# Performance work log

Measured on AMD Instinct MI355X. Metric: run time of the kernel, lower is better.

Reference implementation:

```python
import jax, jax.numpy as jnp
import numpy as np

B, H, W, C = 4, 64, 64, 512
DQK = C // 8


def setup_inputs() -> dict:
    key = jax.random.key(0)
    k1, k2, k3, k4 = jax.random.split(key, 4)
    x = jax.random.normal(k1, (B, H, W, C), dtype=jnp.float32)
    kernel_f = jax.random.normal(k2, (1, 1, C, DQK), dtype=jnp.float32) * 0.02
    kernel_g = jax.random.normal(k3, (1, 1, C, DQK), dtype=jnp.float32) * 0.02
    kernel_h = jax.random.normal(k4, (1, 1, C, C), dtype=jnp.float32) * 0.02
    gamma = jnp.ones((1,), dtype=jnp.float32)  # nonzero so attention branch contributes
    return {"x": x, "kernel_f": kernel_f, "kernel_g": kernel_g,
            "kernel_h": kernel_h, "gamma": gamma}


def reference(x, kernel_f, kernel_g, kernel_h, gamma):
    b, h, w, c = x.shape
    n = h * w
    xt = x.reshape(b, n, c)  # 1x1 conv == per-pixel matmul
    f = jnp.einsum('bnc,cd->bnd', xt, kernel_f[0, 0])       # [b,n,dqk]
    g = jnp.einsum('bnc,cd->bnd', xt, kernel_g[0, 0])       # [b,n,dqk]
    v = jnp.einsum('bnc,cd->bnd', xt, kernel_h[0, 0])       # [b,n,c]
    s = jnp.einsum('bid,bjd->bij', f, g)                    # [b,n,n] = f @ g^T
    beta = jax.nn.softmax(s, axis=-1)
    out = jnp.einsum('bij,bjc->bic', beta, v)               # [b,n,c]
    out = out.reshape(b, h, w, c)
    return gamma * out + x
```

## Files before the change

kernel.cpp:

```cpp
#include <hip/hip_runtime.h>


typedef __bf16 bf16x8 __attribute__((ext_vector_type(8)));
typedef __bf16 bf16x2 __attribute__((ext_vector_type(2)));
typedef float f32x4 __attribute__((ext_vector_type(4)));
typedef unsigned int u32x4 __attribute__((ext_vector_type(4)));
typedef unsigned int u32;

#define L2E 1.4426950408889634f

__device__ __forceinline__ unsigned short f2bf(float f) {
    unsigned int u = __builtin_bit_cast(unsigned int, f);
    u += 0x7fffu + ((u >> 16) & 1u);
    return (unsigned short)(u >> 16);
}
__device__ __forceinline__ u32 cvtpk(float a, float b) {
    bf16x2 t; t[0] = (__bf16)a; t[1] = (__bf16)b;
    return __builtin_bit_cast(u32, t);
}
__device__ __forceinline__ bf16x8 ld8(const void* p) {
    u32x4 u = *reinterpret_cast<const u32x4*>(p);
    return __builtin_bit_cast(bf16x8, u);
}
__device__ __forceinline__ bf16x8 ldx(const float* p) {
    float4 a = *reinterpret_cast<const float4*>(p);
    float4 b = *reinterpret_cast<const float4*>(p + 4);
    u32x4 r;
    r.x = cvtpk(a.x, a.y); r.y = cvtpk(a.z, a.w);
    r.z = cvtpk(b.x, b.y); r.w = cvtpk(b.z, b.w);
    return __builtin_bit_cast(bf16x8, r);
}
__device__ __forceinline__ f32x4 mfma16(bf16x8 a, bf16x8 b, f32x4 c) {
    return __builtin_amdgcn_mfma_f32_16x16x32_bf16(a, b, c, 0, 0, 0);
}
__device__ __forceinline__ void gl2lds16(const void* g, void* l) {
    __builtin_amdgcn_global_load_lds(
        (const __attribute__((address_space(1))) u32*)g,
        (__attribute__((address_space(3))) u32*)l, 16, 0, 0);
}

__global__ __launch_bounds__(256) void cvt_w_all(const float* __restrict__ kf,
                                                 const float* __restrict__ kg,
                                                 const float* __restrict__ kh,
                                                 unsigned short* __restrict__ wst) {
    int idx = blockIdx.x * 256 + threadIdx.x;
    int j = idx & 7;
    int gi = idx >> 3;
    int c = gi % 640;
    int sq = gi / 640;
    int k = (sq >> 2) * 32 + (sq & 3) * 8 + j;
    float v;
    if (c < 64)       v = kf[k * 64 + c] * L2E;
    else if (c < 128) v = kg[k * 64 + (c - 64)];
    else              v = kh[k * 512 + (c - 128)];
    wst[idx] = f2bf(v);
}

__global__ __launch_bounds__(256, 2) void proj_k(const float* __restrict__ x,
                                                 const unsigned short* __restrict__ wst,
                                                 unsigned short* __restrict__ fq,
                                                 unsigned short* __restrict__ kst,
                                                 unsigned short* __restrict__ vst) {
    __shared__ __align__(16) unsigned char Wl[2][20480];
    __shared__ unsigned short Tl[64][72];

    int m0 = blockIdx.x * 64;
    int grp = blockIdx.y;
    int tid = threadIdx.x;
    int w = tid >> 6, l = tid & 63, g = l >> 4, i = l & 15;

    const char* wsrc = (const char*)wst + (size_t)w * 10240 + (size_t)grp * 5120 + l * 16;

#pragma unroll
    for (int s5 = 0; s5 < 5; s5++)
        gl2lds16(wsrc + s5 * 1024, &Wl[0][w * 5120 + s5 * 1024]);

    const float* xrow = x + (size_t)(m0 + 16 * w + i) * 512 + g * 8;
    bf16x8 af[16];
#pragma unroll
    for (int k = 0; k < 16; k++) af[k] = ldx(xrow + 32 * k);

    f32x4 acc[5][4];
#pragma unroll
    for (int t = 0; t < 5; t++)
#pragma unroll
        for (int cf = 0; cf < 4; cf++) acc[t][cf] = f32x4{0, 0, 0, 0};

    int rdoff = g * 5120 + i * 16;

#pragma unroll
    for (int q = 0; q < 16; q++) {
        __syncthreads();
        if (q < 15) {
            const char* src = wsrc + (size_t)(q + 1) * 40960;
#pragma unroll
            for (int s5 = 0; s5 < 5; s5++)
                gl2lds16(src + s5 * 1024, &Wl[(q + 1) & 1][w * 5120 + s5 * 1024]);
        }
        const unsigned char* Wb = &Wl[q & 1][0];
        __builtin_amdgcn_s_setprio(1);
#pragma unroll
        for (int t = 0; t < 5; t++)
#pragma unroll
            for (int cf = 0; cf < 4; cf++) {
                bf16x8 bb = ld8(Wb + rdoff + (t * 64 + 16 * cf) * 16);
                acc[t][cf] = mfma16(af[q], bb, acc[t][cf]);
            }
        __builtin_amdgcn_s_setprio(0);
    }

    int batch = m0 >> 12;
    int kt = (m0 & 4095) >> 6;
    unsigned short* kbase = kst + (size_t)batch * 262144 + (size_t)kt * 4096;
    unsigned short* vbase = vst + (size_t)batch * 2097152 + (size_t)kt * 32768;

#pragma unroll
    for (int t = 0; t < 5; t++) {
        if (grp == 0 && t == 0) {
#pragma unroll
            for (int cf = 0; cf < 4; cf++)
#pragma unroll
                for (int r = 0; r < 4; r++)
                    fq[(size_t)(m0 + 16 * w + 4 * g + r) * 64 + 16 * cf + i] =
                        f2bf(acc[t][cf][r]);
        } else {
            __syncthreads();
#pragma unroll
            for (int cf = 0; cf < 4; cf++) {
                ushort4 v4;
                v4.x = f2bf(acc[t][cf][0]); v4.y = f2bf(acc[t][cf][1]);
                v4.z = f2bf(acc[t][cf][2]); v4.w = f2bf(acc[t][cf][3]);
                *reinterpret_cast<ushort4*>(&Tl[16 * cf + i][16 * w + 4 * g]) = v4;
            }
            __syncthreads();
            if (grp == 0 && t == 1) {
#pragma unroll
                for (int ch = tid; ch < 512; ch += 256) {
                    int jf2 = ch >> 7, ks = (ch >> 6) & 1, l2 = ch & 63;
                    int g2 = l2 >> 4, i2 = l2 & 15;
                    ushort4 o0, o1;
                    o0.x = Tl[ks * 32 + 8 * g2 + 0][16 * jf2 + i2];
                    o0.y = Tl[ks * 32 + 8 * g2 + 1][16 * jf2 + i2];
                    o0.z = Tl[ks * 32 + 8 * g2 + 2][16 * jf2 + i2];
                    o0.w = Tl[ks * 32 + 8 * g2 + 3][16 * jf2 + i2];
                    o1.x = Tl[ks * 32 + 8 * g2 + 4][16 * jf2 + i2];
                    o1.y = Tl[ks * 32 + 8 * g2 + 5][16 * jf2 + i2];
                    o1.z = Tl[ks * 32 + 8 * g2 + 6][16 * jf2 + i2];
                    o1.w = Tl[ks * 32 + 8 * g2 + 7][16 * jf2 + i2];
                    unsigned short* dst = kbase + (size_t)(jf2 * 1024 + ks * 512 + l2 * 8);
                    *reinterpret_cast<ushort4*>(dst)     = o0;
                    *reinterpret_cast<ushort4*>(dst + 4) = o1;
                }
            } else {
                int n0 = (grp == 0) ? (t - 2) * 64 : 192 + t * 64;
#pragma unroll
                for (int ch = tid; ch < 512; ch += 256) {
                    int cc = ch >> 7, ks = (ch >> 6) & 1, l2 = ch & 63;
                    int g2 = l2 >> 4, i2 = l2 & 15;
                    int row = cc * 16 + i2;
                    int jb = 32 * ks + 4 * g2;
                    ushort4 o0, o1;
                    o0.x = Tl[row][jb + 0];  o0.y = Tl[row][jb + 1];
                    o0.z = Tl[row][jb + 2];  o0.w = Tl[row][jb + 3];
                    o1.x = Tl[row][jb + 16]; o1.y = Tl[row][jb + 17];
                    o1.z = Tl[row][jb + 18]; o1.w = Tl[row][jb + 19];
                    int c16 = (n0 >> 4) + cc;
                    unsigned short* dst = vbase + (size_t)(c16 * 1024 + ks * 512 + l2 * 8);
                    *reinterpret_cast<ushort4*>(dst)     = o0;
                    *reinterpret_cast<ushort4*>(dst + 4) = o1;
                }
            }
        }
    }
}

__global__ __launch_bounds__(512, 2) void attn_k(const unsigned short* __restrict__ fq,
                                                 const unsigned short* __restrict__ kst,
                                                 const unsigned short* __restrict__ vst,
                                                 const float* __restrict__ x,
                                                 const float* __restrict__ gamma,
                                                 float* __restrict__ out) {
    __shared__ __align__(16) unsigned char Pl[4][8192];
    __shared__ float l_lds[64];

    int bid = blockIdx.x;
    int xcd = bid & 7;
    int batch = xcd >> 1;
    int qidx = ((xcd & 1) << 5) | (bid >> 3);
    int q0 = qidx * 64;

    int tid = threadIdx.x;
    int w = tid >> 6, l = tid & 63, g = l >> 4, i = l & 15;
    int jf = w >> 1, qfh = w & 1;

    if (tid < 64) l_lds[tid] = 0.0f;

    const unsigned short* fqb = fq + (size_t)batch * 4096 * 64;
    const char* kb = (const char*)kst + (size_t)batch * 524288;
    const char* vb = (const char*)vst + (size_t)batch * 4194304;

    bf16x8 aQ[2][2];
#pragma unroll
    for (int qf_l = 0; qf_l < 2; qf_l++)
#pragma unroll
        for (int ks = 0; ks < 2; ks++)
            aQ[qf_l][ks] = ld8(fqb + (size_t)(q0 + 16 * (2 * qfh + qf_l) + i) * 64 +
                               ks * 32 + g * 8);

    f32x4 acc[4][4];
#pragma unroll
    for (int a = 0; a < 4; a++)
#pragma unroll
        for (int b = 0; b < 4; b++) acc[a][b] = f32x4{0, 0, 0, 0};
    float lp[2] = {0.0f, 0.0f};

    int pwoff = ((2 * qfh) * 2 + (jf >> 1)) * 1024 + l * 16 + (jf & 1) * 8;
    int c16w = w * 4;

    bf16x8 kAa[2], kAb[2];
    kAa[0] = ld8(kb + (size_t)jf * 2048 + l * 16);
    kAa[1] = ld8(kb + (size_t)jf * 2048 + 1024 + l * 16);
    kAb[0] = ld8(kb + (size_t)(4 + jf) * 2048 + l * 16);
    kAb[1] = ld8(kb + (size_t)(4 + jf) * 2048 + 1024 + l * 16);

    bf16x8 vbr_a[4][2], vbr_b[4][2];
#pragma unroll
    for (int cf = 0; cf < 4; cf++)
#pragma unroll
        for (int ks = 0; ks < 2; ks++) {
            vbr_a[cf][ks] = ld8(vb + (size_t)(c16w + cf) * 2048 + ks * 1024 + l * 16);
            vbr_b[cf][ks] = ld8(vb + (size_t)(32 + c16w + cf) * 2048 + ks * 1024 + l * 16);
        }

    {
        f32x4 s0[2] = {f32x4{0,0,0,0}, f32x4{0,0,0,0}};
        f32x4 s1[2] = {f32x4{0,0,0,0}, f32x4{0,0,0,0}};
#pragma unroll
        for (int qf_l = 0; qf_l < 2; qf_l++) {
            s0[qf_l] = mfma16(kAa[0], aQ[qf_l][0], s0[qf_l]);
            s0[qf_l] = mfma16(kAa[1], aQ[qf_l][1], s0[qf_l]);
            s1[qf_l] = mfma16(kAb[0], aQ[qf_l][0], s1[qf_l]);
            s1[qf_l] = mfma16(kAb[1], aQ[qf_l][1], s1[qf_l]);
        }
        kAa[0] = ld8(kb + (size_t)(8 + jf) * 2048 + l * 16);
        kAa[1] = ld8(kb + (size_t)(8 + jf) * 2048 + 1024 + l * 16);
        kAb[0] = ld8(kb + (size_t)(12 + jf) * 2048 + l * 16);
        kAb[1] = ld8(kb + (size_t)(12 + jf) * 2048 + 1024 + l * 16);
#pragma unroll
        for (int qf_l = 0; qf_l < 2; qf_l++) {
            float p0 = __builtin_amdgcn_exp2f(s0[qf_l][0]);
            float p1 = __builtin_amdgcn_exp2f(s0[qf_l][1]);
            float p2 = __builtin_amdgcn_exp2f(s0[qf_l][2]);
            float p3 = __builtin_amdgcn_exp2f(s0[qf_l][3]);
            lp[qf_l] += (p0 + p1) + (p2 + p3);
            uint2 pk2; pk2.x = cvtpk(p0, p1); pk2.y = cvtpk(p2, p3);
            *reinterpret_cast<uint2*>(&Pl[0][0] + pwoff + qf_l * 2048) = pk2;
            p0 = __builtin_amdgcn_exp2f(s1[qf_l][0]);
            p1 = __builtin_amdgcn_exp2f(s1[qf_l][1]);
            p2 = __builtin_amdgcn_exp2f(s1[qf_l][2]);
            p3 = __builtin_amdgcn_exp2f(s1[qf_l][3]);
            lp[qf_l] += (p0 + p1) + (p2 + p3);
            pk2.x = cvtpk(p0, p1); pk2.y = cvtpk(p2, p3);
            *reinterpret_cast<uint2*>(&Pl[1][0] + pwoff + qf_l * 2048) = pk2;
        }
    }

    for (int u = 0; u < 32; ++u) {
        asm volatile("s_waitcnt lgkmcnt(0)" ::: "memory");
        __builtin_amdgcn_s_barrier();

        const unsigned char* Pr0 = &Pl[(u & 1) * 2][0];
        const unsigned char* Pr1 = Pr0 + 8192;

        f32x4 s0[2] = {f32x4{0,0,0,0}, f32x4{0,0,0,0}};
        f32x4 s1[2] = {f32x4{0,0,0,0}, f32x4{0,0,0,0}};
#pragma unroll
        for (int qf_l = 0; qf_l < 2; qf_l++) {
            s0[qf_l] = mfma16(kAa[0], aQ[qf_l][0], s0[qf_l]);
            s0[qf_l] = mfma16(kAa[1], aQ[qf_l][1], s0[qf_l]);
            s1[qf_l] = mfma16(kAb[0], aQ[qf_l][0], s1[qf_l]);
            s1[qf_l] = mfma16(kAb[1], aQ[qf_l][1], s1[qf_l]);
        }

        {
            int ta = (2 * u + 4) & 63, tb = (2 * u + 5) & 63;
            const char* ka = kb + (size_t)(ta * 4 + jf) * 2048;
            const char* kp = kb + (size_t)(tb * 4 + jf) * 2048;
            kAa[0] = ld8(ka + l * 16);
            kAa[1] = ld8(ka + 1024 + l * 16);
            kAb[0] = ld8(kp + l * 16);
            kAb[1] = ld8(kp + 1024 + l * 16);
        }

        {
            bf16x8 aP[4][2];
#pragma unroll
            for (int qf = 0; qf < 4; qf++)
#pragma unroll
                for (int ks = 0; ks < 2; ks++)
                    aP[qf][ks] = ld8(Pr0 + (qf * 2 + ks) * 1024 + l * 16);
            __builtin_amdgcn_s_setprio(1);
#pragma unroll
            for (int cf = 0; cf < 4; cf++)
#pragma unroll
                for (int qf = 0; qf < 4; qf++) {
                    acc[qf][cf] = mfma16(aP[qf][0], vbr_a[cf][0], acc[qf][cf]);
                    acc[qf][cf] = mfma16(aP[qf][1], vbr_a[cf][1], acc[qf][cf]);
                }
            __builtin_amdgcn_s_setprio(0);
        }
        {
            int tv = (2 * u + 2) & 63;
#pragma unroll
            for (int cf = 0; cf < 4; cf++)
#pragma unroll
                for (int ks = 0; ks < 2; ks++)
                    vbr_a[cf][ks] = ld8(vb + (size_t)(tv * 32 + c16w + cf) * 2048 +
                                        ks * 1024 + l * 16);
        }

        {
            bf16x8 aP[4][2];
#pragma unroll
            for (int qf = 0; qf < 4; qf++)
#pragma unroll
                for (int ks = 0; ks < 2; ks++)
                    aP[qf][ks] = ld8(Pr1 + (qf * 2 + ks) * 1024 + l * 16);
            __builtin_amdgcn_s_setprio(1);
#pragma unroll
            for (int cf = 0; cf < 4; cf++)
#pragma unroll
                for (int qf = 0; qf < 4; qf++) {
                    acc[qf][cf] = mfma16(aP[qf][0], vbr_b[cf][0], acc[qf][cf]);
                    acc[qf][cf] = mfma16(aP[qf][1], vbr_b[cf][1], acc[qf][cf]);
                }
            __builtin_amdgcn_s_setprio(0);
        }
        {
            int tv = (2 * u + 3) & 63;
#pragma unroll
            for (int cf = 0; cf < 4; cf++)
#pragma unroll
                for (int ks = 0; ks < 2; ks++)
                    vbr_b[cf][ks] = ld8(vb + (size_t)(tv * 32 + c16w + cf) * 2048 +
                                        ks * 1024 + l * 16);
        }

        float msk = (u < 31) ? 1.0f : 0.0f;
        unsigned char* Pw0 = &Pl[((u + 1) & 1) * 2][0];
        unsigned char* Pw1 = Pw0 + 8192;
#pragma unroll
        for (int qf_l = 0; qf_l < 2; qf_l++) {
            float p0 = __builtin_amdgcn_exp2f(s0[qf_l][0]);
            float p1 = __builtin_amdgcn_exp2f(s0[qf_l][1]);
            float p2 = __builtin_amdgcn_exp2f(s0[qf_l][2]);
            float p3 = __builtin_amdgcn_exp2f(s0[qf_l][3]);
            lp[qf_l] += msk * ((p0 + p1) + (p2 + p3));
            uint2 pk2; pk2.x = cvtpk(p0, p1); pk2.y = cvtpk(p2, p3);
            *reinterpret_cast<uint2*>(Pw0 + pwoff + qf_l * 2048) = pk2;
            p0 = __builtin_amdgcn_exp2f(s1[qf_l][0]);
            p1 = __builtin_amdgcn_exp2f(s1[qf_l][1]);
            p2 = __builtin_amdgcn_exp2f(s1[qf_l][2]);
            p3 = __builtin_amdgcn_exp2f(s1[qf_l][3]);
            lp[qf_l] += msk * ((p0 + p1) + (p2 + p3));
            pk2.x = cvtpk(p0, p1); pk2.y = cvtpk(p2, p3);
            *reinterpret_cast<uint2*>(Pw1 + pwoff + qf_l * 2048) = pk2;
        }
    }

#pragma unroll
    for (int qf_l = 0; qf_l < 2; qf_l++) {
        lp[qf_l] += __shfl_xor(lp[qf_l], 16, 64);
        lp[qf_l] += __shfl_xor(lp[qf_l], 32, 64);
    }
    if (g == 0) {
        atomicAdd(&l_lds[16 * (2 * qfh + 0) + i], lp[0]);
        atomicAdd(&l_lds[16 * (2 * qfh + 1) + i], lp[1]);
    }
    __syncthreads();

    float gam = gamma[0];
#pragma unroll
    for (int qf = 0; qf < 4; qf++) {
#pragma unroll
        for (int r = 0; r < 4; r++) {
            float linv = gam / l_lds[16 * qf + 4 * g + r];
            int n = q0 + 16 * qf + 4 * g + r;
            size_t base = ((size_t)batch * 4096 + n) * 512 + 64 * w;
#pragma unroll
            for (int cf = 0; cf < 4; cf++)
                out[base + 16 * cf + i] = acc[qf][cf][r] * linv + x[base + 16 * cf + i];
        }
    }
}


extern "C" void kernel_launch(void* const* d_in, const int* in_sizes, int n_in,
                              void* d_out, int out_size, void* d_ws, size_t ws_size,
                              hipStream_t stream) {
    const float* x = (const float*)d_in[0];
    const float* kf = (const float*)d_in[1];
    const float* kg = (const float*)d_in[2];
    const float* kh = (const float*)d_in[3];
    const float* gamma = (const float*)d_in[4];
    float* out = (float*)d_out;

    char* ws = (char*)d_ws;
    unsigned short* Fq  = (unsigned short*)(ws);
    unsigned short* Kst = (unsigned short*)(ws + 2097152);
    unsigned short* Vst = (unsigned short*)(ws + 4194304);
    unsigned short* Wst = (unsigned short*)(ws + 20971520);

    cvt_w_all<<<1280, 256, 0, stream>>>(kf, kg, kh, Wst);
    proj_k<<<dim3(256, 2), 256, 0, stream>>>(x, Wst, Fq, Kst, Vst);
    attn_k<<<256, 512, 0, stream>>>(Fq, Kst, Vst, x, gamma, out);
}
```

Baseline: 109.8 us.

## Split attention waves into QK/softmax producers and PV consumers

The attention kernel now gives waves 0-3 the job of computing the QK^T scores, exp and row sums, writing P into double-buffered LDS. Waves 4-7 do only the P·V MFMAs over 128 channels each and write the epilogue. The aim is to let softmax and score work overlap with the PV matrix work on different waves, instead of interleaving them in every wave. In exchange, each consumer wave holds a 4x8 accumulator tile plus a single V register buffer that is reloaded right after use. Under the launch bounds this could cause register spills or expose V load latency, and producer and consumer workloads are unbalanced.

```diff
diff --git a/kernel.cpp b/kernel.cpp
--- a/kernel.cpp
+++ b/kernel.cpp
@@ -121,7 +121,7 @@
             for (int cf = 0; cf < 4; cf++)
 #pragma unroll
                 for (int r = 0; r < 4; r++)
-                    fq[(size_t)(m0 + 16 * w + 4 * g + r) * 64 + 16 * cf + i] =
+                    fq[(size_t)(m0 + 16 * w + 4 * g + r) * 64 + t * 64 + 16 * cf + i] =
                         f2bf(acc[t][cf][r]);
         } else {
             __syncthreads();
@@ -191,205 +191,209 @@
 
     int tid = threadIdx.x;
     int w = tid >> 6, l = tid & 63, g = l >> 4, i = l & 15;
-    int jf = w >> 1, qfh = w & 1;
-
-    if (tid < 64) l_lds[tid] = 0.0f;
 
     const unsigned short* fqb = fq + (size_t)batch * 4096 * 64;
     const char* kb = (const char*)kst + (size_t)batch * 524288;
     const char* vb = (const char*)vst + (size_t)batch * 4194304;
 
-    bf16x8 aQ[2][2];
-#pragma unroll
-    for (int qf_l = 0; qf_l < 2; qf_l++)
+    if (w < 4) {
+        int qf = w;
+        bf16x8 aQ[2];
 #pragma unroll
         for (int ks = 0; ks < 2; ks++)
-            aQ[qf_l][ks] = ld8(fqb + (size_t)(q0 + 16 * (2 * qfh + qf_l) + i) * 64 +
-                               ks * 32 + g * 8);
-
-    f32x4 acc[4][4];
-#pragma unroll
-    for (int a = 0; a < 4; a++)
-#pragma unroll
-        for (int b = 0; b < 4; b++) acc[a][b] = f32x4{0, 0, 0, 0};
-    float lp[2] = {0.0f, 0.0f};
-
-    int pwoff = ((2 * qfh) * 2 + (jf >> 1)) * 1024 + l * 16 + (jf & 1) * 8;
-    int c16w = w * 4;
-
-    bf16x8 kAa[2], kAb[2];
-    kAa[0] = ld8(kb + (size_t)jf * 2048 + l * 16);
-    kAa[1] = ld8(kb + (size_t)jf * 2048 + 1024 + l * 16);
-    kAb[0] = ld8(kb + (size_t)(4 + jf) * 2048 + l * 16);
-    kAb[1] = ld8(kb + (size_t)(4 + jf) * 2048 + 1024 + l * 16);
-
-    bf16x8 vbr_a[4][2], vbr_b[4][2];
-#pragma unroll
-    for (int cf = 0; cf < 4; cf++)
-#pragma unroll
-        for (int ks = 0; ks < 2; ks++) {
-            vbr_a[cf][ks] = ld8(vb + (size_t)(c16w + cf) * 2048 + ks * 1024 + l * 16);
-            vbr_b[cf][ks] = ld8(vb + (size_t)(32 + c16w + cf) * 2048 + ks * 1024 + l * 16);
-        }
-
-    {
-        f32x4 s0[2] = {f32x4{0,0,0,0}, f32x4{0,0,0,0}};
-        f32x4 s1[2] = {f32x4{0,0,0,0}, f32x4{0,0,0,0}};
-#pragma unroll
-        for (int qf_l = 0; qf_l < 2; qf_l++) {
-            s0[qf_l] = mfma16(kAa[0], aQ[qf_l][0], s0[qf_l]);
-            s0[qf_l] = mfma16(kAa[1], aQ[qf_l][1], s0[qf_l]);
-            s1[qf_l] = mfma16(kAb[0], aQ[qf_l][0], s1[qf_l]);
-            s1[qf_l] = mfma16(kAb[1], aQ[qf_l][1], s1[qf_l]);
-        }
-        kAa[0] = ld8(kb + (size_t)(8 + jf) * 2048 + l * 16);
-        kAa[1] = ld8(kb + (size_t)(8 + jf) * 2048 + 1024 + l * 16);
-        kAb[0] = ld8(kb + (size_t)(12 + jf) * 2048 + l * 16);
-        kAb[1] = ld8(kb + (size_t)(12 + jf) * 2048 + 1024 + l * 16);
-#pragma unroll
-        for (int qf_l = 0; qf_l < 2; qf_l++) {
-            float p0 = __builtin_amdgcn_exp2f(s0[qf_l][0]);
-            float p1 = __builtin_amdgcn_exp2f(s0[qf_l][1]);
-            float p2 = __builtin_amdgcn_exp2f(s0[qf_l][2]);
-            float p3 = __builtin_amdgcn_exp2f(s0[qf_l][3]);
-            lp[qf_l] += (p0 + p1) + (p2 + p3);
-            uint2 pk2; pk2.x = cvtpk(p0, p1); pk2.y = cvtpk(p2, p3);
-            *reinterpret_cast<uint2*>(&Pl[0][0] + pwoff + qf_l * 2048) = pk2;
-            p0 = __builtin_amdgcn_exp2f(s1[qf_l][0]);
-            p1 = __builtin_amdgcn_exp2f(s1[qf_l][1]);
-            p2 = __builtin_amdgcn_exp2f(s1[qf_l][2]);
-            p3 = __builtin_amdgcn_exp2f(s1[qf_l][3]);
-            lp[qf_l] += (p0 + p1) + (p2 + p3);
-            pk2.x = cvtpk(p0, p1); pk2.y = cvtpk(p2, p3);
-            *reinterpret_cast<uint2*>(&Pl[1][0] + pwoff + qf_l * 2048) = pk2;
-        }
-    }
-
-    for (int u = 0; u < 32; ++u) {
-        asm volatile("s_waitcnt lgkmcnt(0)" ::: "memory");
-        __builtin_amdgcn_s_barrier();
-
-        const unsigned char* Pr0 = &Pl[(u & 1) * 2][0];
-        const unsigned char* Pr1 = Pr0 + 8192;
-
-        f32x4 s0[2] = {f32x4{0,0,0,0}, f32x4{0,0,0,0}};
-        f32x4 s1[2] = {f32x4{0,0,0,0}, f32x4{0,0,0,0}};
-#pragma unroll
-        for (int qf_l = 0; qf_l < 2; qf_l++) {
-            s0[qf_l] = mfma16(kAa[0], aQ[qf_l][0], s0[qf_l]);
-            s0[qf_l] = mfma16(kAa[1], aQ[qf_l][1], s0[qf_l]);
-            s1[qf_l] = mfma16(kAb[0], aQ[qf_l][0], s1[qf_l]);
-            s1[qf_l] = mfma16(kAb[1], aQ[qf_l][1], s1[qf_l]);
-        }
+            aQ[ks] = ld8(fqb + (size_t)(q0 + 16 * qf + i) * 64 + ks * 32 + g * 8);
+
+        bf16x8 kAa[4][2], kAb[4][2];
+#pragma unroll
+        for (int jf = 0; jf < 4; jf++)
+#pragma unroll
+            for (int ks = 0; ks < 2; ks++) {
+                kAa[jf][ks] = ld8(kb + (size_t)(0 * 4 + jf) * 2048 + ks * 1024 + l * 16);
+                kAb[jf][ks] = ld8(kb + (size_t)(1 * 4 + jf) * 2048 + ks * 1024 + l * 16);
+            }
+
+        float lp = 0.0f;
+        int pw[4];
+#pragma unroll
+        for (int jf = 0; jf < 4; jf++)
+            pw[jf] = (qf * 2 + (jf >> 1)) * 1024 + l * 16 + (jf & 1) * 8;
 
         {
-            int ta = (2 * u + 4) & 63, tb = (2 * u + 5) & 63;
-            const char* ka = kb + (size_t)(ta * 4 + jf) * 2048;
-            const char* kp = kb + (size_t)(tb * 4 + jf) * 2048;
-            kAa[0] = ld8(ka + l * 16);
-            kAa[1] = ld8(ka + 1024 + l * 16);
-            kAb[0] = ld8(kp + l * 16);
-            kAb[1] = ld8(kp + 1024 + l * 16);
-        }
-
-        {
-            bf16x8 aP[4][2];
-#pragma unroll
-            for (int qf = 0; qf < 4; qf++)
-#pragma unroll
-                for (int ks = 0; ks < 2; ks++)
-                    aP[qf][ks] = ld8(Pr0 + (qf * 2 + ks) * 1024 + l * 16);
-            __builtin_amdgcn_s_setprio(1);
-#pragma unroll
-            for (int cf = 0; cf < 4; cf++)
-#pragma unroll
-                for (int qf = 0; qf < 4; qf++) {
-                    acc[qf][cf] = mfma16(aP[qf][0], vbr_a[cf][0], acc[qf][cf]);
-                    acc[qf][cf] = mfma16(aP[qf][1], vbr_a[cf][1], acc[qf][cf]);
+            f32x4 s0[4], s1[4];
+#pragma unroll
+            for (int jf = 0; jf < 4; jf++) { s0[jf] = f32x4{0,0,0,0}; s1[jf] = f32x4{0,0,0,0}; }
+#pragma unroll
+            for (int jf = 0; jf < 4; jf++) {
+                s0[jf] = mfma16(kAa[jf][0], aQ[0], s0[jf]);
+                s0[jf] = mfma16(kAa[jf][1], aQ[1], s0[jf]);
+                s1[jf] = mfma16(kAb[jf][0], aQ[0], s1[jf]);
+                s1[jf] = mfma16(kAb[jf][1], aQ[1], s1[jf]);
+            }
+#pragma unroll
+            for (int jf = 0; jf < 4; jf++)
+#pragma unroll
+                for (int ks = 0; ks < 2; ks++) {
+                    kAa[jf][ks] = ld8(kb + (size_t)(2 * 4 + jf) * 2048 + ks * 1024 + l * 16);
+                    kAb[jf][ks] = ld8(kb + (size_t)(3 * 4 + jf) * 2048 + ks * 1024 + l * 16);
                 }
-            __builtin_amdgcn_s_setprio(0);
-        }
-        {
-            int tv = (2 * u + 2) & 63;
-#pragma unroll
-            for (int cf = 0; cf < 4; cf++)
-#pragma unroll
-                for (int ks = 0; ks < 2; ks++)
-                    vbr_a[cf][ks] = ld8(vb + (size_t)(tv * 32 + c16w + cf) * 2048 +
-                                        ks * 1024 + l * 16);
-        }
-
-        {
-            bf16x8 aP[4][2];
-#pragma unroll
-            for (int qf = 0; qf < 4; qf++)
-#pragma unroll
-                for (int ks = 0; ks < 2; ks++)
-                    aP[qf][ks] = ld8(Pr1 + (qf * 2 + ks) * 1024 + l * 16);
-            __builtin_amdgcn_s_setprio(1);
-#pragma unroll
-            for (int cf = 0; cf < 4; cf++)
-#pragma unroll
-                for (int qf = 0; qf < 4; qf++) {
-                    acc[qf][cf] = mfma16(aP[qf][0], vbr_b[cf][0], acc[qf][cf]);
-                    acc[qf][cf] = mfma16(aP[qf][1], vbr_b[cf][1], acc[qf][cf]);
+#pragma unroll
+            for (int jf = 0; jf < 4; jf++) {
+                float p0 = __builtin_amdgcn_exp2f(s0[jf][0]);
+                float p1 = __builtin_amdgcn_exp2f(s0[jf][1]);
+                float p2 = __builtin_amdgcn_exp2f(s0[jf][2]);
+                float p3 = __builtin_amdgcn_exp2f(s0[jf][3]);
+                lp += (p0 + p1) + (p2 + p3);
+                uint2 pk2; pk2.x = cvtpk(p0, p1); pk2.y = cvtpk(p2, p3);
+                *reinterpret_cast<uint2*>(&Pl[0][0] + pw[jf]) = pk2;
+                p0 = __builtin_amdgcn_exp2f(s1[jf][0]);
+                p1 = __builtin_amdgcn_exp2f(s1[jf][1]);
+                p2 = __builtin_amdgcn_exp2f(s1[jf][2]);
+                p3 = __builtin_amdgcn_exp2f(s1[jf][3]);
+                lp += (p0 + p1) + (p2 + p3);
+                pk2.x = cvtpk(p0, p1); pk2.y = cvtpk(p2, p3);
+                *reinterpret_cast<uint2*>(&Pl[1][0] + pw[jf]) = pk2;
+            }
+        }
+
+        for (int u = 0; u < 32; ++u) {
+            asm volatile("s_waitcnt lgkmcnt(0)" ::: "memory");
+            __builtin_amdgcn_s_barrier();
+
+            f32x4 s0[4], s1[4];
+#pragma unroll
+            for (int jf = 0; jf < 4; jf++) { s0[jf] = f32x4{0,0,0,0}; s1[jf] = f32x4{0,0,0,0}; }
+#pragma unroll
+            for (int jf = 0; jf < 4; jf++) {
+                s0[jf] = mfma16(kAa[jf][0], aQ[0], s0[jf]);
+                s0[jf] = mfma16(kAa[jf][1], aQ[1], s0[jf]);
+                s1[jf] = mfma16(kAb[jf][0], aQ[0], s1[jf]);
+                s1[jf] = mfma16(kAb[jf][1], aQ[1], s1[jf]);
+            }
+
+            {
+                int ta = (2 * u + 4) & 63, tb = (2 * u + 5) & 63;
+#pragma unroll
+                for (int jf = 0; jf < 4; jf++)
+#pragma unroll
+                    for (int ks = 0; ks < 2; ks++) {
+                        kAa[jf][ks] = ld8(kb + (size_t)(ta * 4 + jf) * 2048 + ks * 1024 + l * 16);
+                        kAb[jf][ks] = ld8(kb + (size_t)(tb * 4 + jf) * 2048 + ks * 1024 + l * 16);
+                    }
+            }
+
+            float msk = (u < 31) ? 1.0f : 0.0f;
+            unsigned char* Pw0 = &Pl[((u + 1) & 1) * 2][0];
+            unsigned char* Pw1 = Pw0 + 8192;
+#pragma unroll
+            for (int jf = 0; jf < 4; jf++) {
+                float p0 = __builtin_amdgcn_exp2f(s0[jf][0]);
+                float p1 = __builtin_amdgcn_exp2f(s0[jf][1]);
+                float p2 = __builtin_amdgcn_exp2f(s0[jf][2]);
+                float p3 = __builtin_amdgcn_exp2f(s0[jf][3]);
+                lp += msk * ((p0 + p1) + (p2 + p3));
+                uint2 pk2; pk2.x = cvtpk(p0, p1); pk2.y = cvtpk(p2, p3);
+                *reinterpret_cast<uint2*>(Pw0 + pw[jf]) = pk2;
+                p0 = __builtin_amdgcn_exp2f(s1[jf][0]);
+                p1 = __builtin_amdgcn_exp2f(s1[jf][1]);
+                p2 = __builtin_amdgcn_exp2f(s1[jf][2]);
+                p3 = __builtin_amdgcn_exp2f(s1[jf][3]);
+                lp += msk * ((p0 + p1) + (p2 + p3));
+                pk2.x = cvtpk(p0, p1); pk2.y = cvtpk(p2, p3);
+                *reinterpret_cast<uint2*>(Pw1 + pw[jf]) = pk2;
+            }
+        }
+
+        lp += __shfl_xor(lp, 16, 64);
+        lp += __shfl_xor(lp, 32, 64);
+        if (g == 0) l_lds[16 * qf + i] = lp;
+        __syncthreads();
+    } else {
+        int p = w - 4;
+        int c16b = 8 * p;
+
+        bf16x8 vbr[8][2];
+#pragma unroll
+        for (int cf = 0; cf < 8; cf++)
+#pragma unroll
+            for (int ks = 0; ks < 2; ks++)
+                vbr[cf][ks] = ld8(vb + (size_t)(c16b + cf) * 2048 + ks * 1024 + l * 16);
+
+        f32x4 acc[4][8];
+#pragma unroll
+        for (int a = 0; a < 4; a++)
+#pragma unroll
+            for (int b = 0; b < 8; b++) acc[a][b] = f32x4{0, 0, 0, 0};
+
+        for (int u = 0; u < 32; ++u) {
+            asm volatile("s_waitcnt lgkmcnt(0)" ::: "memory");
+            __builtin_amdgcn_s_barrier();
+
+            const unsigned char* Pr0 = &Pl[(u & 1) * 2][0];
+            const unsigned char* Pr1 = Pr0 + 8192;
+
+            {
+                bf16x8 aP[4][2];
+#pragma unroll
+                for (int qf = 0; qf < 4; qf++)
+#pragma unroll
+                    for (int ks = 0; ks < 2; ks++)
+                        aP[qf][ks] = ld8(Pr0 + (qf * 2 + ks) * 1024 + l * 16);
+                int tv = (2 * u + 1) & 63;
+                __builtin_amdgcn_s_setprio(1);
+#pragma unroll
+                for (int cf = 0; cf < 8; cf++) {
+#pragma unroll
+                    for (int qf = 0; qf < 4; qf++) {
+                        acc[qf][cf] = mfma16(aP[qf][0], vbr[cf][0], acc[qf][cf]);
+                        acc[qf][cf] = mfma16(aP[qf][1], vbr[cf][1], acc[qf][cf]);
+                    }
+#pragma unroll
+                    for (int ks = 0; ks < 2; ks++)
+                        vbr[cf][ks] = ld8(vb + (size_t)(tv * 32 + c16b + cf) * 2048 +
+                                          ks * 1024 + l * 16);
                 }
-            __builtin_amdgcn_s_setprio(0);
-        }
-        {
-            int tv = (2 * u + 3) & 63;
-#pragma unroll
-            for (int cf = 0; cf < 4; cf++)
-#pragma unroll
-                for (int ks = 0; ks < 2; ks++)
-                    vbr_b[cf][ks] = ld8(vb + (size_t)(tv * 32 + c16w + cf) * 2048 +
-                                        ks * 1024 + l * 16);
-        }
-
-        float msk = (u < 31) ? 1.0f : 0.0f;
-        unsigned char* Pw0 = &Pl[((u + 1) & 1) * 2][0];
-        unsigned char* Pw1 = Pw0 + 8192;
-#pragma unroll
-        for (int qf_l = 0; qf_l < 2; qf_l++) {
-            float p0 = __builtin_amdgcn_exp2f(s0[qf_l][0]);
-            float p1 = __builtin_amdgcn_exp2f(s0[qf_l][1]);
-            float p2 = __builtin_amdgcn_exp2f(s0[qf_l][2]);
-            float p3 = __builtin_amdgcn_exp2f(s0[qf_l][3]);
-            lp[qf_l] += msk * ((p0 + p1) + (p2 + p3));
-            uint2 pk2; pk2.x = cvtpk(p0, p1); pk2.y = cvtpk(p2, p3);
-            *reinterpret_cast<uint2*>(Pw0 + pwoff + qf_l * 2048) = pk2;
-            p0 = __builtin_amdgcn_exp2f(s1[qf_l][0]);
-            p1 = __builtin_amdgcn_exp2f(s1[qf_l][1]);
-            p2 = __builtin_amdgcn_exp2f(s1[qf_l][2]);
-            p3 = __builtin_amdgcn_exp2f(s1[qf_l][3]);
-            lp[qf_l] += msk * ((p0 + p1) + (p2 + p3));
-            pk2.x = cvtpk(p0, p1); pk2.y = cvtpk(p2, p3);
-            *reinterpret_cast<uint2*>(Pw1 + pwoff + qf_l * 2048) = pk2;
-        }
-    }
-
-#pragma unroll
-    for (int qf_l = 0; qf_l < 2; qf_l++) {
-        lp[qf_l] += __shfl_xor(lp[qf_l], 16, 64);
-        lp[qf_l] += __shfl_xor(lp[qf_l], 32, 64);
-    }
-    if (g == 0) {
-        atomicAdd(&l_lds[16 * (2 * qfh + 0) + i], lp[0]);
-        atomicAdd(&l_lds[16 * (2 * qfh + 1) + i], lp[1]);
-    }
-    __syncthreads();
-
-    float gam = gamma[0];
-#pragma unroll
-    for (int qf = 0; qf < 4; qf++) {
-#pragma unroll
-        for (int r = 0; r < 4; r++) {
-            float linv = gam / l_lds[16 * qf + 4 * g + r];
-            int n = q0 + 16 * qf + 4 * g + r;
-            size_t base = ((size_t)batch * 4096 + n) * 512 + 64 * w;
-#pragma unroll
-            for (int cf = 0; cf < 4; cf++)
-                out[base + 16 * cf + i] = acc[qf][cf][r] * linv + x[base + 16 * cf + i];
+                __builtin_amdgcn_s_setprio(0);
+            }
+
+            {
+                bf16x8 aP[4][2];
+#pragma unroll
+                for (int qf = 0; qf < 4; qf++)
+#pragma unroll
+                    for (int ks = 0; ks < 2; ks++)
+                        aP[qf][ks] = ld8(Pr1 + (qf * 2 + ks) * 1024 + l * 16);
+                int tv = (2 * u + 2) & 63;
+                __builtin_amdgcn_s_setprio(1);
+#pragma unroll
+                for (int cf = 0; cf < 8; cf++) {
+#pragma unroll
+                    for (int qf = 0; qf < 4; qf++) {
+                        acc[qf][cf] = mfma16(aP[qf][0], vbr[cf][0], acc[qf][cf]);
+                        acc[qf][cf] = mfma16(aP[qf][1], vbr[cf][1], acc[qf][cf]);
+                    }
+#pragma unroll
+                    for (int ks = 0; ks < 2; ks++)
+                        vbr[cf][ks] = ld8(vb + (size_t)(tv * 32 + c16b + cf) * 2048 +
+                                          ks * 1024 + l * 16);
+                }
+                __builtin_amdgcn_s_setprio(0);
+            }
+        }
+
+        __syncthreads();
+
+        float gam = gamma[0];
+#pragma unroll
+        for (int qf = 0; qf < 4; qf++) {
+#pragma unroll
+            for (int r = 0; r < 4; r++) {
+                float linv = gam / l_lds[16 * qf + 4 * g + r];
+                int n = q0 + 16 * qf + 4 * g + r;
+                size_t base = ((size_t)batch * 4096 + n) * 512 + 128 * p;
+#pragma unroll
+                for (int cf = 0; cf < 8; cf++)
+                    out[base + 16 * cf + i] = acc[qf][cf][r] * linv + x[base + 16 * cf + i];
+            }
         }
     }
 }
```

New measurement: 111.1 us. About the same (+1.2%).
